# Performance work log

Measured on AMD Instinct MI355X. Metric: run time of the kernel, lower is better.

The kernel has to match this reference:

```python
import jax, jax.numpy as jnp
import numpy as np

N = 100000
E = 1600000
NFEAT, NHID, NCLASS = 128, 64, 40
EPS = 1e-5


def _sage_conv(x, src, dst, wl, wr, b):
    # mean aggregation over in-neighbors: out[dst] = mean_{src->dst} x[src]
    msg = jax.ops.segment_sum(x[src], dst, num_segments=N)          # [N, d]
    deg = jax.ops.segment_sum(jnp.ones((src.shape[0],), x.dtype), dst, num_segments=N)
    agg = msg / jnp.maximum(deg, 1.0)[:, None]
    return agg @ wl + x @ wr + b


def _bn_eval(x, g, b, m, v):
    return (x - m) * (g * jax.lax.rsqrt(v + EPS)) + b


def setup_inputs() -> dict:
    key = jax.random.key(0)
    ks = jax.random.split(key, 12)
    s = 0.05
    x = jax.random.normal(ks[0], (N, NFEAT), dtype=jnp.float32)
    edge_index = jax.random.randint(ks[1], (2, E), 0, N, dtype=jnp.int64)
    inp = {
        'x': x,
        'edge_index': edge_index,
        'w1l': jax.random.normal(ks[2], (NFEAT, NHID), jnp.float32) * s,
        'w1r': jax.random.normal(ks[3], (NFEAT, NHID), jnp.float32) * s,
        'b1': jnp.zeros((NHID,), jnp.float32),
        'wxl': jax.random.normal(ks[4], (NHID, NHID), jnp.float32) * s,
        'wxr': jax.random.normal(ks[5], (NHID, NHID), jnp.float32) * s,
        'bx': jnp.zeros((NHID,), jnp.float32),
        'w2l': jax.random.normal(ks[6], (NHID, NCLASS), jnp.float32) * s,
        'w2r': jax.random.normal(ks[7], (NHID, NCLASS), jnp.float32) * s,
        'b2': jnp.zeros((NCLASS,), jnp.float32),
        'bn3_g': jnp.ones((NHID,), jnp.float32),
        'bn3_b': jnp.zeros((NHID,), jnp.float32),
        'bn3_m': jax.random.normal(ks[8], (NHID,), jnp.float32) * 0.1,
        'bn3_v': jax.random.uniform(ks[9], (NHID,), jnp.float32, 0.5, 1.5),
        'bn2_g': jnp.ones((NCLASS,), jnp.float32),
        'bn2_b': jnp.zeros((NCLASS,), jnp.float32),
        'bn2_m': jax.random.normal(ks[10], (NCLASS,), jnp.float32) * 0.1,
        'bn2_v': jax.random.uniform(ks[11], (NCLASS,), jnp.float32, 0.5, 1.5),
    }
    return inp


def reference(x, edge_index, w1l, w1r, b1, wxl, wxr, bx, w2l, w2r, b2,
              bn3_g, bn3_b, bn3_m, bn3_v, bn2_g, bn2_b, bn2_m, bn2_v):
    src, dst = edge_index[0], edge_index[1]
    h = jax.nn.relu(_sage_conv(x, src, dst, w1l, w1r, b1))          # conv1 + relu
    # middle layer (layer=3 -> one convx iteration); dropout = identity (eval)
    h = _sage_conv(h, src, dst, wxl, wxr, bx)
    h = jax.nn.relu(_bn_eval(h, bn3_g, bn3_b, bn3_m, bn3_v))
    # final layer
    h = _sage_conv(h, src, dst, w2l, w2r, b2)
    return _bn_eval(h, bn2_g, bn2_b, bn2_m, bn2_v)                  # [N, NCLASS]
```

## Files before the change

### kernel.cpp

```cpp
#include <hip/hip_runtime.h>

#define NNODES 100000
#define NEDGES 1600000
#define NBK    196
#define BK_CAP 9000
#define BKP    17024
#define CHUNK  4096
#define ZOFF   (NNODES * 128)

typedef short bhalf8 __attribute__((ext_vector_type(8)));
typedef float f32x4 __attribute__((ext_vector_type(4)));

__device__ __forceinline__ unsigned fbits(float x){ union{float f;unsigned u;}c; c.f=x; return c.u; }
__device__ __forceinline__ float bcast(unsigned u){ union{float f;unsigned u;}c; c.u=u; return c.f; }
__device__ __forceinline__ unsigned short rtn16(float x){
    unsigned u = fbits(x);
    return (unsigned short)((u + 0x7FFFu + ((u >> 16) & 1u)) >> 16);
}

__global__ void zero_bcur(int* __restrict__ bcur) {
    int t = threadIdx.x;
    if (t < NBK) bcur[t] = 0;
}

__global__ __launch_bounds__(256) void bucketize(
    const int* __restrict__ ei, unsigned* __restrict__ recs, int* __restrict__ bcur) {
    __shared__ int s_is64;
    __shared__ int cnt[256], base[256], loc[256], rnk[256];
    __shared__ unsigned stage[CHUNK];
    __shared__ unsigned char bkof[CHUNK];
    const int t = threadIdx.x;
    if (t < 64) {
        int v = ei[2 * t + 1];
        unsigned long long nz = __ballot(v != 0);
        if (t == 0) s_is64 = (nz == 0ULL) ? 1 : 0;
    }
    cnt[t] = 0; rnk[t] = 0;
    __syncthreads();
    const int is64 = s_is64;
    const long start = (long)blockIdx.x * CHUNK;
    const int2* ei2 = (const int2*)ei;
#pragma unroll
    for (int k = 0; k < CHUNK / 256; ++k) {
        long e = start + k * 256 + t;
        if (e < NEDGES) {
            int d = is64 ? ei2[NEDGES + e].x : ei[NEDGES + e];
            atomicAdd(&cnt[d >> 9], 1);
        }
    }
    __syncthreads();
    int v = cnt[t];
    int run = v;
    loc[t] = run;
    __syncthreads();
    for (int off = 1; off < 256; off <<= 1) {
        int other = (t >= off) ? loc[t - off] : 0;
        __syncthreads();
        run += other;
        loc[t] = run;
        __syncthreads();
    }
    int excl = run - v;
    if (v > 0) base[t] = atomicAdd(&bcur[t], v);
    loc[t] = excl;
    __syncthreads();
#pragma unroll
    for (int k = 0; k < CHUNK / 256; ++k) {
        long e = start + k * 256 + t;
        if (e < NEDGES) {
            int s = is64 ? ei2[e].x : ei[e];
            int d = is64 ? ei2[NEDGES + e].x : ei[NEDGES + e];
            int b = d >> 9;
            int r = atomicAdd(&rnk[b], 1);
            int pos = loc[b] + r;
            stage[pos] = ((unsigned)s << 9) | (unsigned)(d & 511);
            bkof[pos] = (unsigned char)b;
        }
    }
    __syncthreads();
    const int tot = (int)min((long)CHUNK, NEDGES - start);
    for (int i = t; i < tot; i += 256) {
        int b = bkof[i];
        int pos = base[b] + (i - loc[b]);
        if (pos < BK_CAP)
            recs[(size_t)b * BK_CAP + pos] = stage[i];
    }
}

__global__ __launch_bounds__(512) void csr_build(
    const unsigned* __restrict__ recs, const int* __restrict__ bcur,
    int2* __restrict__ offs2, int* __restrict__ degs, int* __restrict__ csr) {
    const int b = blockIdx.x;
    const int t = threadIdx.x;
    const int lo = b << 9;
    __shared__ int sc[512];
    __shared__ int hist[512];
    __shared__ int lstart[512];
    const int n = bcur[b];
    const unsigned* P = recs + (size_t)b * BK_CAP;
    hist[t] = 0;
    __syncthreads();
    for (int i = t; i < n; i += 512)
        atomicAdd(&hist[P[i] & 511], 1);
    __syncthreads();
    const int deg = hist[t];
    const int pad = (deg + 15) & ~15;
    int run = pad;
    sc[t] = run;
    __syncthreads();
    for (int off = 1; off < 512; off <<= 1) {
        int other = (t >= off) ? sc[t - off] : 0;
        __syncthreads();
        run += other;
        sc[t] = run;
        __syncthreads();
    }
    const int start = b * BKP + (run - pad);
    lstart[t] = start;
    const int node = lo + t;
    if (node < NNODES) {
        offs2[node] = make_int2(start, start + pad);
        degs[node] = deg;
    }
    hist[t] = 0;
    __syncthreads();
    for (int i = t; i < n; i += 512) {
        unsigned rec = P[i];
        int d = rec & 511;
        int r = atomicAdd(&hist[d], 1);
        csr[lstart[d] + r] = (int)(rec >> 9) * 128;
    }
    __syncthreads();
    for (int i = deg; i < pad; ++i)
        csr[start + i] = ZOFF;
}

template <int K, int NL, int NTOT>
__device__ __forceinline__ void prep_section(
    int blk, int nblk, const float* wl, const float* wr, const float* bias,
    const float* g, const float* bb, const float* m, const float* vv,
    unsigned short* Bh, unsigned short* Bl, float* bfix) {
    constexpr int NCT = NTOT / 16;
    constexpr int TOT = (K / 32) * NCT * 512;
    int tid = blk * 256 + threadIdx.x;
    if (tid < NL) {
        float sc = g ? g[tid] * rsqrtf(vv[tid] + 1e-5f) : 1.f;
        float sh = g ? (bb[tid] - m[tid] * sc) : 0.f;
        bfix[tid] = bias[tid] * sc + sh;
    }
    for (int idx = tid; idx < TOT; idx += nblk * 256) {
        int e = idx & 7, l = (idx >> 3) & 63, rest = idx >> 9;
        int ct = rest % NCT, kc = rest / NCT;
        int k = kc * 32 + (l >> 4) * 8 + e;
        int j = ct * 16 + (l & 15);
        int jj = (j < NL) ? j : j - NL;
        float sc = g ? g[jj] * rsqrtf(vv[jj] + 1e-5f) : 1.f;
        float v = ((j < NL) ? wl[k * NL + j] : wr[k * NL + (j - NL)]) * sc;
        unsigned short h = rtn16(v);
        float r1 = v - bcast((unsigned)h << 16);
        Bh[idx] = h;
        Bl[idx] = rtn16(r1);
    }
}

__global__ __launch_bounds__(256) void prep_all(
    const float* w1l, const float* w1r, const float* b1,
    const float* wxl, const float* wxr, const float* bx,
    const float* w2l, const float* w2r, const float* b2,
    const float* g3, const float* bb3, const float* m3, const float* v3,
    const float* g2, const float* bb2, const float* m2, const float* v2,
    unsigned short* B1h, unsigned short* B1l, float* bf1,
    unsigned short* B2h, unsigned short* B2l, float* bf2,
    unsigned short* B3h, unsigned short* B3l, float* bf3) {
    int blk = blockIdx.x;
    if (blk < 64)
        prep_section<128, 64, 128>(blk, 64, w1l, w1r, b1,
                                   nullptr, nullptr, nullptr, nullptr, B1h, B1l, bf1);
    else if (blk < 96)
        prep_section<64, 64, 128>(blk - 64, 32, wxl, wxr, bx,
                                  g3, bb3, m3, v3, B2h, B2l, bf2);
    else
        prep_section<64, 40, 80>(blk - 96, 20, w2l, w2r, b2,
                                 g2, bb2, m2, v2, B3h, B3l, bf3);
}

template <int K, int NL, int NTOT, bool ABF16>
__global__ __launch_bounds__(256, 2) void gemm_mfma(
    const void* __restrict__ hvp, const unsigned short* __restrict__ Bh,
    const unsigned short* __restrict__ Bl, const float* __restrict__ bias,
    unsigned short* __restrict__ zl, unsigned short* __restrict__ zr, int nrows) {
    constexpr int NCT = NTOT / 16;
    constexpr int NKC = K / 32;
    constexpr int TOT = NKC * NCT * 512;
    __shared__ unsigned short Bs[2 * TOT];
    int t = threadIdx.x;
    int l = t & 63, w = t >> 6;
    int rb = blockIdx.x * 64 + w * 16;
    int arow = rb + (l & 15);
    int kg = l >> 4;
    const bool aok = (arow < nrows);
    bhalf8 ah_r[NKC], al_r[NKC];
    float4 a0[NKC], a1[NKC];
#pragma unroll
    for (int kc = 0; kc < NKC; ++kc) {
        if (ABF16) {
            const unsigned short* hr =
                (const unsigned short*)hvp + (long)arow * K + kg * 8;
            ah_r[kc] = (bhalf8){0,0,0,0,0,0,0,0};
            if (aok) ah_r[kc] = *(const bhalf8*)(hr + kc * 32);
        } else {
            const float* hr = (const float*)hvp + (long)arow * K + kg * 8;
            a0[kc] = make_float4(0.f, 0.f, 0.f, 0.f); a1[kc] = a0[kc];
            if (aok) {
                a0[kc] = *(const float4*)(hr + kc * 32);
                a1[kc] = *(const float4*)(hr + kc * 32 + 4);
            }
        }
    }
    {
        const uint4* gh = (const uint4*)Bh;
        const uint4* gl = (const uint4*)Bl;
        uint4* sh = (uint4*)Bs;
        uint4* sl = (uint4*)(Bs + TOT);
#pragma unroll 2
        for (int i = t; i < TOT / 8; i += 256) { sh[i] = gh[i]; sl[i] = gl[i]; }
    }
    __syncthreads();
    if (!ABF16) {
#pragma unroll
        for (int kc = 0; kc < NKC; ++kc) {
            float av[8] = {a0[kc].x, a0[kc].y, a0[kc].z, a0[kc].w,
                           a1[kc].x, a1[kc].y, a1[kc].z, a1[kc].w};
#pragma unroll
            for (int e = 0; e < 8; ++e) {
                unsigned short hh = rtn16(av[e]);
                float r1 = av[e] - bcast((unsigned)hh << 16);
                ah_r[kc][e] = (short)hh;
                al_r[kc][e] = (short)rtn16(r1);
            }
        }
    }
    f32x4 acc[NCT];
#pragma unroll
    for (int ct = 0; ct < NCT; ++ct) acc[ct] = (f32x4){0.f, 0.f, 0.f, 0.f};
#pragma unroll
    for (int kc = 0; kc < NKC; ++kc) {
#pragma unroll
        for (int ct = 0; ct < NCT; ++ct) {
            bhalf8 bh = *(const bhalf8*)&Bs[(kc * NCT + ct) * 512 + l * 8];
            bhalf8 bl2 = *(const bhalf8*)&Bs[TOT + (kc * NCT + ct) * 512 + l * 8];
            acc[ct] = __builtin_amdgcn_mfma_f32_16x16x32_bf16(ah_r[kc], bh, acc[ct], 0, 0, 0);
            acc[ct] = __builtin_amdgcn_mfma_f32_16x16x32_bf16(ah_r[kc], bl2, acc[ct], 0, 0, 0);
            if (!ABF16)
                acc[ct] = __builtin_amdgcn_mfma_f32_16x16x32_bf16(al_r[kc], bh, acc[ct], 0, 0, 0);
        }
    }
    int orow0 = rb + kg * 4;
#pragma unroll
    for (int ct = 0; ct < NCT; ++ct) {
        int j = ct * 16 + (l & 15);
        bool isl = (j < NL);
        int cc = isl ? j : j - NL;
        float bj = isl ? 0.f : bias[cc];
#pragma unroll
        for (int r = 0; r < 4; ++r) {
            int orow = orow0 + r;
            if (orow < nrows) {
                if (isl) zl[(long)orow * 64 + cc] = rtn16(acc[ct][r]);
                else     zr[(long)orow * NL + cc] = rtn16(acc[ct][r] + bj);
            } else if (orow == nrows && isl) {
                zl[(long)orow * 64 + cc] = 0;
            }
        }
    }
}

template <int NOUT, bool RELU, typename OUTT>
__global__ __launch_bounds__(256) void combine_kernel(
    const unsigned short* __restrict__ zl, const unsigned short* __restrict__ zr,
    const int2* __restrict__ offs2, const int* __restrict__ degs,
    const int* __restrict__ csr, OUTT* __restrict__ out) {
    int wid  = (blockIdx.x * blockDim.x + threadIdx.x) >> 6;
    int lane = threadIdx.x & 63;
    if (wid >= NNODES) return;
    int q    = lane >> 5;
    int li2  = (lane & 31) * 2;
    unsigned lib = (unsigned)li2 * 2;
    const char* zlb = (const char*)zl;
    unsigned uzr = *(const unsigned*)&zr[(long)wid * NOUT + li2];
    float zr0 = bcast(uzr << 16), zr1 = bcast(uzr & 0xFFFF0000u);
    float invd = 1.f / fmaxf((float)degs[wid], 1.f);
    int2 se = offs2[wid];
    float ax = 0.f, ay = 0.f;
    for (int base = se.x; base < se.y; base += 64) {
        int c = min(64, se.y - base);
        int sv = csr[base + lane];
        for (int p0 = 0; p0 < c; p0 += 16) {
            unsigned hv[8];
#pragma unroll
            for (int j = 0; j < 8; ++j) {
                unsigned soff = (unsigned)__shfl(sv, p0 + 2 * j + q);
                hv[j] = *(const unsigned*)(zlb + soff + lib);
            }
#pragma unroll
            for (int j = 0; j < 8; ++j) {
                ax += bcast(hv[j] << 16);
                ay += bcast(hv[j] & 0xFFFF0000u);
            }
        }
    }
    ax += __shfl_xor(ax, 32);
    ay += __shfl_xor(ay, 32);
    if (q != 0 || li2 >= NOUT) return;
    float r0 = ax * invd + zr0;
    float r1 = ay * invd + zr1;
    if (RELU) { r0 = fmaxf(r0, 0.f); r1 = fmaxf(r1, 0.f); }
    if constexpr (sizeof(OUTT) == 4) {
        *(float2*)&out[(long)wid * NOUT + li2] = make_float2(r0, r1);
    } else {
        *(ushort2*)&out[(long)wid * NOUT + li2] = make_ushort2(rtn16(r0), rtn16(r1));
    }
}

extern "C" void kernel_launch(void* const* d_in, const int* in_sizes, int n_in,
                              void* d_out, int out_size, void* d_ws, size_t ws_size,
                              hipStream_t stream) {
    const float* x    = (const float*)d_in[0];
    const int*   ei   = (const int*)d_in[1];
    const float* w1l  = (const float*)d_in[2];
    const float* w1r  = (const float*)d_in[3];
    const float* b1   = (const float*)d_in[4];
    const float* wxl  = (const float*)d_in[5];
    const float* wxr  = (const float*)d_in[6];
    const float* bx   = (const float*)d_in[7];
    const float* w2l  = (const float*)d_in[8];
    const float* w2r  = (const float*)d_in[9];
    const float* b2   = (const float*)d_in[10];
    const float* bn3g = (const float*)d_in[11];
    const float* bn3b = (const float*)d_in[12];
    const float* bn3m = (const float*)d_in[13];
    const float* bn3v = (const float*)d_in[14];
    const float* bn2g = (const float*)d_in[15];
    const float* bn2b = (const float*)d_in[16];
    const float* bn2m = (const float*)d_in[17];
    const float* bn2v = (const float*)d_in[18];
    float* out = (float*)d_out;

    char* p = (char*)d_ws;
    auto alloc = [&](size_t bytes) -> void* {
        void* r = (void*)p;
        p += (bytes + 255) & ~(size_t)255;
        return r;
    };
    int*   bcur  = (int*)alloc(NBK * 4);
    int2*  offs2 = (int2*)alloc((size_t)NNODES * 8);
    int*   degs  = (int*)alloc((size_t)NNODES * 4);
    int*   csr   = (int*)alloc(((size_t)NBK * BKP + 64) * 4);
    unsigned short* h16  = (unsigned short*)alloc((size_t)NNODES * 64 * 2);
    unsigned short* zl16 = (unsigned short*)alloc((size_t)(NNODES + 1) * 64 * 2);
    unsigned short* zr16 = (unsigned short*)alloc((size_t)NNODES * 64 * 2);
    unsigned short* B1h = (unsigned short*)alloc(16384 * 2);
    unsigned short* B1l = (unsigned short*)alloc(16384 * 2);
    unsigned short* B2h = (unsigned short*)alloc(8192 * 2);
    unsigned short* B2l = (unsigned short*)alloc(8192 * 2);
    unsigned short* B3h = (unsigned short*)alloc(5120 * 2);
    unsigned short* B3l = (unsigned short*)alloc(5120 * 2);
    float* bfix1 = (float*)alloc(64 * 4);
    float* bfix2 = (float*)alloc(64 * 4);
    float* bfix3 = (float*)alloc(40 * 4);
    unsigned* recs = (unsigned*)h16;

    zero_bcur<<<1, 256, 0, stream>>>(bcur);
    bucketize<<<(NEDGES + CHUNK - 1) / CHUNK, 256, 0, stream>>>(ei, recs, bcur);
    prep_all<<<116, 256, 0, stream>>>(w1l, w1r, b1, wxl, wxr, bx, w2l, w2r, b2,
                                      bn3g, bn3b, bn3m, bn3v, bn2g, bn2b, bn2m, bn2v,
                                      B1h, B1l, bfix1, B2h, B2l, bfix2, B3h, B3l, bfix3);
    csr_build<<<NBK, 512, 0, stream>>>(recs, bcur, offs2, degs, csr);

    const int GB = (NNODES + 63) / 64;
    gemm_mfma<128, 64, 128, false><<<GB, 256, 0, stream>>>(x, B1h, B1l, bfix1, zl16, zr16, NNODES);
    combine_kernel<64, true, unsigned short><<<25000, 256, 0, stream>>>(
        zl16, zr16, offs2, degs, csr, h16);
    gemm_mfma<64, 64, 128, true><<<GB, 256, 0, stream>>>(h16, B2h, B2l, bfix2, zl16, zr16, NNODES);
    combine_kernel<64, true, unsigned short><<<25000, 256, 0, stream>>>(
        zl16, zr16, offs2, degs, csr, h16);
    gemm_mfma<64, 40, 80, true><<<GB, 256, 0, stream>>>(h16, B3h, B3l, bfix3, zl16, zr16, NNODES);
    combine_kernel<40, false, float><<<25000, 256, 0, stream>>>(
        zl16, zr16, offs2, degs, csr, out);
}
```

Baseline: 216.0 us.

## Process four row groups per GEMM block with double-buffered A prefetch

Each GEMM block now handles 256 rows instead of 64, so the B weight tiles staged into shared memory are reused across four row groups and are loaded from global memory four times less often in total. A fragments for the next group are prefetched into registers while the current group's MFMAs run. The launch-bounds occupancy hint is dropped, and the extra register buffers may lower occupancy. The grid shrinks to about 391 blocks, which may leave compute units underused.

```diff
diff --git a/kernel.cpp b/kernel.cpp
--- a/kernel.cpp
+++ b/kernel.cpp
@@ -185,7 +185,7 @@
 }
 
 template <int K, int NL, int NTOT, bool ABF16>
-__global__ __launch_bounds__(256, 2) void gemm_mfma(
+__global__ __launch_bounds__(256) void gemm_mfma(
     const void* __restrict__ hvp, const unsigned short* __restrict__ Bh,
     const unsigned short* __restrict__ Bl, const float* __restrict__ bias,
     unsigned short* __restrict__ zl, unsigned short* __restrict__ zr, int nrows) {
@@ -195,25 +195,30 @@
     __shared__ unsigned short Bs[2 * TOT];
     int t = threadIdx.x;
     int l = t & 63, w = t >> 6;
-    int rb = blockIdx.x * 64 + w * 16;
-    int arow = rb + (l & 15);
+    int rb0 = blockIdx.x * 256 + w * 16;
     int kg = l >> 4;
-    const bool aok = (arow < nrows);
-    bhalf8 ah_r[NKC], al_r[NKC];
-    float4 a0[NKC], a1[NKC];
-#pragma unroll
-    for (int kc = 0; kc < NKC; ++kc) {
+    int rl = l & 15;
+    float4 a0b[2][NKC], a1b[2][NKC];
+    bhalf8 ahb[2][NKC];
+    {
+        int arow = rb0 + rl;
+        bool ok = arow < nrows;
         if (ABF16) {
-            const unsigned short* hr =
-                (const unsigned short*)hvp + (long)arow * K + kg * 8;
-            ah_r[kc] = (bhalf8){0,0,0,0,0,0,0,0};
-            if (aok) ah_r[kc] = *(const bhalf8*)(hr + kc * 32);
+            const unsigned short* hr = (const unsigned short*)hvp + (long)arow * K + kg * 8;
+#pragma unroll
+            for (int kc = 0; kc < NKC; ++kc) {
+                ahb[0][kc] = (bhalf8){0,0,0,0,0,0,0,0};
+                if (ok) ahb[0][kc] = *(const bhalf8*)(hr + kc * 32);
+            }
         } else {
             const float* hr = (const float*)hvp + (long)arow * K + kg * 8;
-            a0[kc] = make_float4(0.f, 0.f, 0.f, 0.f); a1[kc] = a0[kc];
-            if (aok) {
-                a0[kc] = *(const float4*)(hr + kc * 32);
-                a1[kc] = *(const float4*)(hr + kc * 32 + 4);
+#pragma unroll
+            for (int kc = 0; kc < NKC; ++kc) {
+                a0b[0][kc] = make_float4(0.f,0.f,0.f,0.f); a1b[0][kc] = a0b[0][kc];
+                if (ok) {
+                    a0b[0][kc] = *(const float4*)(hr + kc * 32);
+                    a1b[0][kc] = *(const float4*)(hr + kc * 32 + 4);
+                }
             }
         }
     }
@@ -222,54 +227,83 @@
         const uint4* gl = (const uint4*)Bl;
         uint4* sh = (uint4*)Bs;
         uint4* sl = (uint4*)(Bs + TOT);
-#pragma unroll 2
         for (int i = t; i < TOT / 8; i += 256) { sh[i] = gh[i]; sl[i] = gl[i]; }
     }
     __syncthreads();
-    if (!ABF16) {
+#pragma unroll
+    for (int g = 0; g < 4; ++g) {
+        const int cur = g & 1, nxt = cur ^ 1;
+        if (g < 3) {
+            int arow = rb0 + (g + 1) * 64 + rl;
+            bool ok = arow < nrows;
+            if (ABF16) {
+                const unsigned short* hr = (const unsigned short*)hvp + (long)arow * K + kg * 8;
+#pragma unroll
+                for (int kc = 0; kc < NKC; ++kc) {
+                    ahb[nxt][kc] = (bhalf8){0,0,0,0,0,0,0,0};
+                    if (ok) ahb[nxt][kc] = *(const bhalf8*)(hr + kc * 32);
+                }
+            } else {
+                const float* hr = (const float*)hvp + (long)arow * K + kg * 8;
+#pragma unroll
+                for (int kc = 0; kc < NKC; ++kc) {
+                    a0b[nxt][kc] = make_float4(0.f,0.f,0.f,0.f); a1b[nxt][kc] = a0b[nxt][kc];
+                    if (ok) {
+                        a0b[nxt][kc] = *(const float4*)(hr + kc * 32);
+                        a1b[nxt][kc] = *(const float4*)(hr + kc * 32 + 4);
+                    }
+                }
+            }
+        }
+        bhalf8 ah[NKC], al[NKC];
+        if (ABF16) {
+#pragma unroll
+            for (int kc = 0; kc < NKC; ++kc) ah[kc] = ahb[cur][kc];
+        } else {
+#pragma unroll
+            for (int kc = 0; kc < NKC; ++kc) {
+                float av[8] = {a0b[cur][kc].x, a0b[cur][kc].y, a0b[cur][kc].z, a0b[cur][kc].w,
+                               a1b[cur][kc].x, a1b[cur][kc].y, a1b[cur][kc].z, a1b[cur][kc].w};
+#pragma unroll
+                for (int e = 0; e < 8; ++e) {
+                    unsigned short hh = rtn16(av[e]);
+                    float r1 = av[e] - bcast((unsigned)hh << 16);
+                    ah[kc][e] = (short)hh;
+                    al[kc][e] = (short)rtn16(r1);
+                }
+            }
+        }
+        f32x4 acc[NCT];
+#pragma unroll
+        for (int ct = 0; ct < NCT; ++ct) acc[ct] = (f32x4){0.f, 0.f, 0.f, 0.f};
 #pragma unroll
         for (int kc = 0; kc < NKC; ++kc) {
-            float av[8] = {a0[kc].x, a0[kc].y, a0[kc].z, a0[kc].w,
-                           a1[kc].x, a1[kc].y, a1[kc].z, a1[kc].w};
-#pragma unroll
-            for (int e = 0; e < 8; ++e) {
-                unsigned short hh = rtn16(av[e]);
-                float r1 = av[e] - bcast((unsigned)hh << 16);
-                ah_r[kc][e] = (short)hh;
-                al_r[kc][e] = (short)rtn16(r1);
-            }
-        }
-    }
-    f32x4 acc[NCT];
-#pragma unroll
-    for (int ct = 0; ct < NCT; ++ct) acc[ct] = (f32x4){0.f, 0.f, 0.f, 0.f};
-#pragma unroll
-    for (int kc = 0; kc < NKC; ++kc) {
+#pragma unroll
+            for (int ct = 0; ct < NCT; ++ct) {
+                bhalf8 bh = *(const bhalf8*)&Bs[(kc * NCT + ct) * 512 + l * 8];
+                bhalf8 bl2 = *(const bhalf8*)&Bs[TOT + (kc * NCT + ct) * 512 + l * 8];
+                acc[ct] = __builtin_amdgcn_mfma_f32_16x16x32_bf16(ah[kc], bh, acc[ct], 0, 0, 0);
+                acc[ct] = __builtin_amdgcn_mfma_f32_16x16x32_bf16(ah[kc], bl2, acc[ct], 0, 0, 0);
+                if (!ABF16)
+                    acc[ct] = __builtin_amdgcn_mfma_f32_16x16x32_bf16(al[kc], bh, acc[ct], 0, 0, 0);
+            }
+        }
+        int orow0 = rb0 + g * 64 + kg * 4;
 #pragma unroll
         for (int ct = 0; ct < NCT; ++ct) {
-            bhalf8 bh = *(const bhalf8*)&Bs[(kc * NCT + ct) * 512 + l * 8];
-            bhalf8 bl2 = *(const bhalf8*)&Bs[TOT + (kc * NCT + ct) * 512 + l * 8];
-            acc[ct] = __builtin_amdgcn_mfma_f32_16x16x32_bf16(ah_r[kc], bh, acc[ct], 0, 0, 0);
-            acc[ct] = __builtin_amdgcn_mfma_f32_16x16x32_bf16(ah_r[kc], bl2, acc[ct], 0, 0, 0);
-            if (!ABF16)
-                acc[ct] = __builtin_amdgcn_mfma_f32_16x16x32_bf16(al_r[kc], bh, acc[ct], 0, 0, 0);
-        }
-    }
-    int orow0 = rb + kg * 4;
-#pragma unroll
-    for (int ct = 0; ct < NCT; ++ct) {
-        int j = ct * 16 + (l & 15);
-        bool isl = (j < NL);
-        int cc = isl ? j : j - NL;
-        float bj = isl ? 0.f : bias[cc];
-#pragma unroll
-        for (int r = 0; r < 4; ++r) {
-            int orow = orow0 + r;
-            if (orow < nrows) {
-                if (isl) zl[(long)orow * 64 + cc] = rtn16(acc[ct][r]);
-                else     zr[(long)orow * NL + cc] = rtn16(acc[ct][r] + bj);
-            } else if (orow == nrows && isl) {
-                zl[(long)orow * 64 + cc] = 0;
+            int j = ct * 16 + rl;
+            bool isl = (j < NL);
+            int cc = isl ? j : j - NL;
+            float bj = isl ? 0.f : bias[cc];
+#pragma unroll
+            for (int r = 0; r < 4; ++r) {
+                int orow = orow0 + r;
+                if (orow < nrows) {
+                    if (isl) zl[(long)orow * 64 + cc] = rtn16(acc[ct][r]);
+                    else     zr[(long)orow * NL + cc] = rtn16(acc[ct][r] + bj);
+                } else if (orow == nrows && isl) {
+                    zl[(long)orow * 64 + cc] = 0;
+                }
             }
         }
     }
@@ -377,7 +411,7 @@
                                       B1h, B1l, bfix1, B2h, B2l, bfix2, B3h, B3l, bfix3);
     csr_build<<<NBK, 512, 0, stream>>>(recs, bcur, offs2, degs, csr);
 
-    const int GB = (NNODES + 63) / 64;
+    const int GB = (NNODES + 255) / 256;
     gemm_mfma<128, 64, 128, false><<<GB, 256, 0, stream>>>(x, B1h, B1l, bfix1, zl16, zr16, NNODES);
     combine_kernel<64, true, unsigned short><<<25000, 256, 0, stream>>>(
         zl16, zr16, offs2, degs, csr, h16);
```

Result: slower. 223.3 us (+3.4%).

## Fuse neighbor aggregation with next-layer GEMM and fold bucket reset into prep

Applied to the files above, without the earlier changes.

Replaces the combine, gemm pairs for layers two and three with one fused kernel. Each block aggregates 64 nodes' neighbor means into shared memory, applies ReLU, then runs the MFMA GEMM on those rows directly. This avoids writing and re-reading the intermediate h16 activations and drops two launches. Weights are read straight from global memory instead of being staged in LDS. Each wave now processes 16 nodes one after another, which gives less gather parallelism per block than one wave per node. The zero_bcur kernel is merged into prep_all as an extra block, and ping-pong z buffers are added.

```diff
diff --git a/kernel.cpp b/kernel.cpp
--- a/kernel.cpp
+++ b/kernel.cpp
@@ -16,11 +16,6 @@
 __device__ __forceinline__ unsigned short rtn16(float x){
     unsigned u = fbits(x);
     return (unsigned short)((u + 0x7FFFu + ((u >> 16) & 1u)) >> 16);
-}
-
-__global__ void zero_bcur(int* __restrict__ bcur) {
-    int t = threadIdx.x;
-    if (t < NBK) bcur[t] = 0;
 }
 
 __global__ __launch_bounds__(256) void bucketize(
@@ -171,7 +166,8 @@
     const float* g2, const float* bb2, const float* m2, const float* v2,
     unsigned short* B1h, unsigned short* B1l, float* bf1,
     unsigned short* B2h, unsigned short* B2l, float* bf2,
-    unsigned short* B3h, unsigned short* B3l, float* bf3) {
+    unsigned short* B3h, unsigned short* B3l, float* bf3,
+    int* bcur) {
     int blk = blockIdx.x;
     if (blk < 64)
         prep_section<128, 64, 128>(blk, 64, w1l, w1r, b1,
@@ -179,42 +175,32 @@
     else if (blk < 96)
         prep_section<64, 64, 128>(blk - 64, 32, wxl, wxr, bx,
                                   g3, bb3, m3, v3, B2h, B2l, bf2);
-    else
+    else if (blk < 116)
         prep_section<64, 40, 80>(blk - 96, 20, w2l, w2r, b2,
                                  g2, bb2, m2, v2, B3h, B3l, bf3);
-}
-
-template <int K, int NL, int NTOT, bool ABF16>
-__global__ __launch_bounds__(256, 2) void gemm_mfma(
-    const void* __restrict__ hvp, const unsigned short* __restrict__ Bh,
+    else {
+        if (threadIdx.x < NBK) bcur[threadIdx.x] = 0;
+    }
+}
+
+__global__ __launch_bounds__(256, 2) void gemm1(
+    const float* __restrict__ x, const unsigned short* __restrict__ Bh,
     const unsigned short* __restrict__ Bl, const float* __restrict__ bias,
     unsigned short* __restrict__ zl, unsigned short* __restrict__ zr, int nrows) {
-    constexpr int NCT = NTOT / 16;
-    constexpr int NKC = K / 32;
-    constexpr int TOT = NKC * NCT * 512;
+    constexpr int NCT = 8, NKC = 4, TOT = NKC * NCT * 512;
     __shared__ unsigned short Bs[2 * TOT];
-    int t = threadIdx.x;
-    int l = t & 63, w = t >> 6;
+    int t = threadIdx.x, l = t & 63, w = t >> 6;
     int rb = blockIdx.x * 64 + w * 16;
-    int arow = rb + (l & 15);
-    int kg = l >> 4;
-    const bool aok = (arow < nrows);
-    bhalf8 ah_r[NKC], al_r[NKC];
+    int arow = rb + (l & 15), kg = l >> 4;
+    const bool aok = arow < nrows;
     float4 a0[NKC], a1[NKC];
+    const float* hr = x + (long)arow * 128 + kg * 8;
 #pragma unroll
     for (int kc = 0; kc < NKC; ++kc) {
-        if (ABF16) {
-            const unsigned short* hr =
-                (const unsigned short*)hvp + (long)arow * K + kg * 8;
-            ah_r[kc] = (bhalf8){0,0,0,0,0,0,0,0};
-            if (aok) ah_r[kc] = *(const bhalf8*)(hr + kc * 32);
-        } else {
-            const float* hr = (const float*)hvp + (long)arow * K + kg * 8;
-            a0[kc] = make_float4(0.f, 0.f, 0.f, 0.f); a1[kc] = a0[kc];
-            if (aok) {
-                a0[kc] = *(const float4*)(hr + kc * 32);
-                a1[kc] = *(const float4*)(hr + kc * 32 + 4);
-            }
+        a0[kc] = make_float4(0.f, 0.f, 0.f, 0.f); a1[kc] = a0[kc];
+        if (aok) {
+            a0[kc] = *(const float4*)(hr + kc * 32);
+            a1[kc] = *(const float4*)(hr + kc * 32 + 4);
         }
     }
     {
@@ -222,22 +208,20 @@
         const uint4* gl = (const uint4*)Bl;
         uint4* sh = (uint4*)Bs;
         uint4* sl = (uint4*)(Bs + TOT);
-#pragma unroll 2
         for (int i = t; i < TOT / 8; i += 256) { sh[i] = gh[i]; sl[i] = gl[i]; }
     }
     __syncthreads();
-    if (!ABF16) {
-#pragma unroll
-        for (int kc = 0; kc < NKC; ++kc) {
-            float av[8] = {a0[kc].x, a0[kc].y, a0[kc].z, a0[kc].w,
-                           a1[kc].x, a1[kc].y, a1[kc].z, a1[kc].w};
-#pragma unroll
-            for (int e = 0; e < 8; ++e) {
-                unsigned short hh = rtn16(av[e]);
-                float r1 = av[e] - bcast((unsigned)hh << 16);
-                ah_r[kc][e] = (short)hh;
-                al_r[kc][e] = (short)rtn16(r1);
-            }
+    bhalf8 ah[NKC], al[NKC];
+#pragma unroll
+    for (int kc = 0; kc < NKC; ++kc) {
+        float av[8] = {a0[kc].x, a0[kc].y, a0[kc].z, a0[kc].w,
+                       a1[kc].x, a1[kc].y, a1[kc].z, a1[kc].w};
+#pragma unroll
+        for (int e = 0; e < 8; ++e) {
+            unsigned short hh = rtn16(av[e]);
+            float r1 = av[e] - bcast((unsigned)hh << 16);
+            ah[kc][e] = (short)hh;
+            al[kc][e] = (short)rtn16(r1);
         }
     }
     f32x4 acc[NCT];
@@ -249,27 +233,119 @@
         for (int ct = 0; ct < NCT; ++ct) {
             bhalf8 bh = *(const bhalf8*)&Bs[(kc * NCT + ct) * 512 + l * 8];
             bhalf8 bl2 = *(const bhalf8*)&Bs[TOT + (kc * NCT + ct) * 512 + l * 8];
-            acc[ct] = __builtin_amdgcn_mfma_f32_16x16x32_bf16(ah_r[kc], bh, acc[ct], 0, 0, 0);
-            acc[ct] = __builtin_amdgcn_mfma_f32_16x16x32_bf16(ah_r[kc], bl2, acc[ct], 0, 0, 0);
-            if (!ABF16)
-                acc[ct] = __builtin_amdgcn_mfma_f32_16x16x32_bf16(al_r[kc], bh, acc[ct], 0, 0, 0);
+            acc[ct] = __builtin_amdgcn_mfma_f32_16x16x32_bf16(ah[kc], bh, acc[ct], 0, 0, 0);
+            acc[ct] = __builtin_amdgcn_mfma_f32_16x16x32_bf16(ah[kc], bl2, acc[ct], 0, 0, 0);
+            acc[ct] = __builtin_amdgcn_mfma_f32_16x16x32_bf16(al[kc], bh, acc[ct], 0, 0, 0);
         }
     }
     int orow0 = rb + kg * 4;
 #pragma unroll
     for (int ct = 0; ct < NCT; ++ct) {
         int j = ct * 16 + (l & 15);
-        bool isl = (j < NL);
-        int cc = isl ? j : j - NL;
+        bool isl = (j < 64);
+        int cc = isl ? j : j - 64;
         float bj = isl ? 0.f : bias[cc];
 #pragma unroll
         for (int r = 0; r < 4; ++r) {
             int orow = orow0 + r;
             if (orow < nrows) {
                 if (isl) zl[(long)orow * 64 + cc] = rtn16(acc[ct][r]);
-                else     zr[(long)orow * NL + cc] = rtn16(acc[ct][r] + bj);
+                else     zr[(long)orow * 64 + cc] = rtn16(acc[ct][r] + bj);
             } else if (orow == nrows && isl) {
                 zl[(long)orow * 64 + cc] = 0;
+            }
+        }
+    }
+}
+
+template <int NL>
+__global__ __launch_bounds__(256) void fused_cg(
+    const unsigned short* __restrict__ zli, const unsigned short* __restrict__ zri,
+    const int2* __restrict__ offs2, const int* __restrict__ degs,
+    const int* __restrict__ csr,
+    const unsigned short* __restrict__ Bh, const unsigned short* __restrict__ Bl,
+    const float* __restrict__ bias,
+    unsigned short* __restrict__ zlo, unsigned short* __restrict__ zro) {
+    constexpr int NCT = (2 * NL) / 16;
+    constexpr int NKC = 2;
+    __shared__ unsigned short hs[64][72];
+    int t = threadIdx.x, l = t & 63, w = t >> 6;
+    int rb = blockIdx.x * 64;
+    int q = l >> 5;
+    int li2 = (l & 31) * 2;
+    unsigned lib = (unsigned)li2 * 2;
+    const char* zlb = (const char*)zli;
+#pragma unroll 1
+    for (int i = 0; i < 16; ++i) {
+        int node = rb + w * 16 + i;
+        float r0 = 0.f, r1 = 0.f;
+        if (node < NNODES) {
+            unsigned uzr = *(const unsigned*)&zri[(long)node * 64 + li2];
+            float zr0 = bcast(uzr << 16), zr1 = bcast(uzr & 0xFFFF0000u);
+            float invd = 1.f / fmaxf((float)degs[node], 1.f);
+            int2 se = offs2[node];
+            float ax = 0.f, ay = 0.f;
+            for (int base = se.x; base < se.y; base += 64) {
+                int c = min(64, se.y - base);
+                int sv = csr[base + l];
+                for (int p0 = 0; p0 < c; p0 += 16) {
+                    unsigned hv[8];
+#pragma unroll
+                    for (int j = 0; j < 8; ++j) {
+                        unsigned soff = (unsigned)__shfl(sv, p0 + 2 * j + q);
+                        hv[j] = *(const unsigned*)(zlb + soff + lib);
+                    }
+#pragma unroll
+                    for (int j = 0; j < 8; ++j) {
+                        ax += bcast(hv[j] << 16);
+                        ay += bcast(hv[j] & 0xFFFF0000u);
+                    }
+                }
+            }
+            ax += __shfl_xor(ax, 32);
+            ay += __shfl_xor(ay, 32);
+            r0 = fmaxf(ax * invd + zr0, 0.f);
+            r1 = fmaxf(ay * invd + zr1, 0.f);
+        }
+        if (q == 0)
+            *(ushort2*)&hs[w * 16 + i][li2] = make_ushort2(rtn16(r0), rtn16(r1));
+    }
+    __syncthreads();
+    int kg = l >> 4, rl = l & 15;
+    bhalf8 ah[NKC];
+#pragma unroll
+    for (int kc = 0; kc < NKC; ++kc)
+        ah[kc] = *(const bhalf8*)&hs[w * 16 + rl][kc * 32 + kg * 8];
+    f32x4 acc[NCT];
+#pragma unroll
+    for (int ct = 0; ct < NCT; ++ct) acc[ct] = (f32x4){0.f, 0.f, 0.f, 0.f};
+#pragma unroll
+    for (int kc = 0; kc < NKC; ++kc) {
+        const unsigned short* hp = Bh + (size_t)(kc * NCT) * 512 + l * 8;
+        const unsigned short* lp = Bl + (size_t)(kc * NCT) * 512 + l * 8;
+#pragma unroll
+        for (int ct = 0; ct < NCT; ++ct) {
+            bhalf8 bh = *(const bhalf8*)(hp + ct * 512);
+            bhalf8 bl2 = *(const bhalf8*)(lp + ct * 512);
+            acc[ct] = __builtin_amdgcn_mfma_f32_16x16x32_bf16(ah[kc], bh, acc[ct], 0, 0, 0);
+            acc[ct] = __builtin_amdgcn_mfma_f32_16x16x32_bf16(ah[kc], bl2, acc[ct], 0, 0, 0);
+        }
+    }
+    int orow0 = rb + w * 16 + kg * 4;
+#pragma unroll
+    for (int ct = 0; ct < NCT; ++ct) {
+        int j = ct * 16 + rl;
+        bool isl = (j < NL);
+        int cc = isl ? j : j - NL;
+        float bj = isl ? 0.f : bias[cc];
+#pragma unroll
+        for (int r = 0; r < 4; ++r) {
+            int orow = orow0 + r;
+            if (orow < NNODES) {
+                if (isl) zlo[(long)orow * 64 + cc] = rtn16(acc[ct][r]);
+                else     zro[(long)orow * NL + cc] = rtn16(acc[ct][r] + bj);
+            } else if (orow == NNODES && isl) {
+                zlo[(long)orow * 64 + cc] = 0;
             }
         }
     }
@@ -356,9 +432,10 @@
     int2*  offs2 = (int2*)alloc((size_t)NNODES * 8);
     int*   degs  = (int*)alloc((size_t)NNODES * 4);
     int*   csr   = (int*)alloc(((size_t)NBK * BKP + 64) * 4);
-    unsigned short* h16  = (unsigned short*)alloc((size_t)NNODES * 64 * 2);
-    unsigned short* zl16 = (unsigned short*)alloc((size_t)(NNODES + 1) * 64 * 2);
-    unsigned short* zr16 = (unsigned short*)alloc((size_t)NNODES * 64 * 2);
+    unsigned short* zlA = (unsigned short*)alloc((size_t)(NNODES + 1) * 64 * 2);
+    unsigned short* zrA = (unsigned short*)alloc((size_t)NNODES * 64 * 2);
+    unsigned short* zlB = (unsigned short*)alloc((size_t)(NNODES + 1) * 64 * 2);
+    unsigned short* zrB = (unsigned short*)alloc((size_t)NNODES * 64 * 2);
     unsigned short* B1h = (unsigned short*)alloc(16384 * 2);
     unsigned short* B1l = (unsigned short*)alloc(16384 * 2);
     unsigned short* B2h = (unsigned short*)alloc(8192 * 2);
@@ -368,23 +445,21 @@
     float* bfix1 = (float*)alloc(64 * 4);
     float* bfix2 = (float*)alloc(64 * 4);
     float* bfix3 = (float*)alloc(40 * 4);
-    unsigned* recs = (unsigned*)h16;
-
-    zero_bcur<<<1, 256, 0, stream>>>(bcur);
+    unsigned* recs = (unsigned*)zlA;
+
+    prep_all<<<117, 256, 0, stream>>>(w1l, w1r, b1, wxl, wxr, bx, w2l, w2r, b2,
+                                      bn3g, bn3b, bn3m, bn3v, bn2g, bn2b, bn2m, bn2v,
+                                      B1h, B1l, bfix1, B2h, B2l, bfix2, B3h, B3l, bfix3,
+                                      bcur);
     bucketize<<<(NEDGES + CHUNK - 1) / CHUNK, 256, 0, stream>>>(ei, recs, bcur);
-    prep_all<<<116, 256, 0, stream>>>(w1l, w1r, b1, wxl, wxr, bx, w2l, w2r, b2,
-                                      bn3g, bn3b, bn3m, bn3v, bn2g, bn2b, bn2m, bn2v,
-                                      B1h, B1l, bfix1, B2h, B2l, bfix2, B3h, B3l, bfix3);
     csr_build<<<NBK, 512, 0, stream>>>(recs, bcur, offs2, degs, csr);
 
     const int GB = (NNODES + 63) / 64;
-    gemm_mfma<128, 64, 128, false><<<GB, 256, 0, stream>>>(x, B1h, B1l, bfix1, zl16, zr16, NNODES);
-    combine_kernel<64, true, unsigned short><<<25000, 256, 0, stream>>>(
-        zl16, zr16, offs2, degs, csr, h16);
-    gemm_mfma<64, 64, 128, true><<<GB, 256, 0, stream>>>(h16, B2h, B2l, bfix2, zl16, zr16, NNODES);
-    combine_kernel<64, true, unsigned short><<<25000, 256, 0, stream>>>(
-        zl16, zr16, offs2, degs, csr, h16);
-    gemm_mfma<64, 40, 80, true><<<GB, 256, 0, stream>>>(h16, B3h, B3l, bfix3, zl16, zr16, NNODES);
+    gemm1<<<GB, 256, 0, stream>>>(x, B1h, B1l, bfix1, zlA, zrA, NNODES);
+    fused_cg<64><<<GB, 256, 0, stream>>>(zlA, zrA, offs2, degs, csr,
+                                         B2h, B2l, bfix2, zlB, zrB);
+    fused_cg<40><<<GB, 256, 0, stream>>>(zlB, zrB, offs2, degs, csr,
+                                         B3h, B3l, bfix3, zlA, zrA);
     combine_kernel<40, false, float><<<25000, 256, 0, stream>>>(
-        zl16, zr16, offs2, degs, csr, out);
-}
+        zlA, zrA, offs2, degs, csr, out);
+}
```

New measurement: 228.8 us. +5.9%, slower.
